# Kernel tuning notes

Measured on AMD Instinct MI355X. Metric: run time of the kernel, lower is better.

Reference implementation:

```python
import jax, jax.numpy as jnp
import numpy as np

NUM_HEADS = 16
B, S, H = 2, 8192, 1024


def setup_inputs() -> dict:
    key = jax.random.key(0)
    ks = jax.random.split(key, 6)
    scale = 1.0 / np.sqrt(H)
    return {
        "hidden_states": jax.random.normal(ks[0], (B, S, H), dtype=jnp.float32),
        "Wq": jax.random.normal(ks[1], (H, H), dtype=jnp.float32) * scale,
        "Wk": jax.random.normal(ks[2], (H, H), dtype=jnp.float32) * scale,
        "Wv": jax.random.normal(ks[3], (H, H), dtype=jnp.float32) * scale,
        "Wg": jax.random.normal(ks[4], (H, H), dtype=jnp.float32) * scale,
        "Wo": jax.random.normal(ks[5], (H, H), dtype=jnp.float32) * scale,
        "gamma": jnp.ones((H,), dtype=jnp.float32),
        "beta": jnp.zeros((H,), dtype=jnp.float32),
    }


def reference(hidden_states, Wq, Wk, Wv, Wg, Wo, gamma, beta):
    b, s, h = hidden_states.shape
    nh = NUM_HEADS
    dk = h // nh
    dv = h // nh
    # projections (bias-free linears)
    q = (hidden_states @ Wq).reshape(b, s, nh, dk)
    k = (hidden_states @ Wk).reshape(b, s, nh, dk)
    v = (hidden_states @ Wv).reshape(b, s, nh, dv)
    g = hidden_states @ Wg  # [b, s, h]
    # elu+1 feature map
    q = jax.nn.elu(q) + 1.0
    k = jax.nn.elu(k) + 1.0
    # kv = k outer v per token, then contracted with q  ==> (q.k) * v (no [b,h,n,d,e] tensor)
    qk = jnp.sum(q * k, axis=-1, keepdims=True)        # [b, s, nh, 1]
    k_sum = jnp.sum(k, axis=1, keepdims=True)          # [b, 1, nh, dk] (global over seq)
    normalizer = jnp.sum(q * k_sum, axis=-1, keepdims=True)  # [b, s, nh, 1]
    z = qk * v / (normalizer + 1e-6)                   # [b, s, nh, dv]
    z = z.reshape(b, s, nh * dv)
    # LayerNorm (eps=1e-5, affine)
    mu = jnp.mean(z, axis=-1, keepdims=True)
    var = jnp.mean(jnp.square(z - mu), axis=-1, keepdims=True)
    z = (z - mu) * jax.lax.rsqrt(var + 1e-5) * gamma + beta
    # SiLU gating and output projection
    z = z * jax.nn.silu(g)
    return z @ Wo
```

## Files before the change

kernel.cpp:

```cpp
#include <hip/hip_runtime.h>


typedef unsigned short ushort_t;
typedef unsigned int uint_t;

using short8  = __attribute__((ext_vector_type(8))) short;
using floatx4 = __attribute__((ext_vector_type(4))) float;

#define HDIM  1024
#define T_TOK 16384
#define KSPLIT 3072

__device__ __forceinline__ ushort_t f2bf(float f) {
    uint_t u = __builtin_bit_cast(uint_t, f);
    u = (u + 0x7fff + ((u >> 16) & 1)) >> 16;
    return (ushort_t)u;
}
__device__ __forceinline__ float bf2f(ushort_t h) {
    uint_t u = ((uint_t)h) << 16;
    return __builtin_bit_cast(float, u);
}
__device__ __forceinline__ void split2(float f, ushort_t& hi, ushort_t& lo) {
    hi = f2bf(f);
    lo = f2bf(f - bf2f(hi));
}
__device__ __forceinline__ void gload_lds16(const ushort_t* g, ushort_t* l) {
    __builtin_amdgcn_global_load_lds(
        (const __attribute__((address_space(1))) void*)g,
        (__attribute__((address_space(3))) void*)l, 16, 0, 0);
}

__global__ void split_w(const float* __restrict__ W0, const float* __restrict__ W1,
                        const float* __restrict__ W2, const float* __restrict__ W3,
                        const float* __restrict__ W4, ushort_t* __restrict__ WT2) {
    __shared__ float tile[32][33];
    const int z = blockIdx.z;
    const float* W = (z == 0) ? W0 : (z == 1) ? W1 : (z == 2) ? W2 : (z == 3) ? W3 : W4;
    ushort_t* dst = WT2 + (size_t)z * HDIM * 2048;
    const int n0 = blockIdx.x * 32, k0 = blockIdx.y * 32;
    const int tx = threadIdx.x & 31, ty0 = threadIdx.x >> 5;
#pragma unroll
    for (int s = 0; s < 4; ++s) {
        int ty = ty0 + 8 * s;
        tile[ty][tx] = W[(size_t)(k0 + ty) * HDIM + n0 + tx];
    }
    __syncthreads();
#pragma unroll
    for (int s = 0; s < 4; ++s) {
        int ty = ty0 + 8 * s;
        float v = tile[tx][ty];
        ushort_t hi, lo;
        split2(v, hi, lo);
        dst[(size_t)(n0 + ty) * 2048 + k0 + tx] = hi;
        dst[(size_t)(n0 + ty) * 2048 + 1024 + k0 + tx] = lo;
    }
}

__global__ __launch_bounds__(256)
void split_hidden(const float* __restrict__ h, ushort_t* __restrict__ Hs) {
    const int t = blockIdx.x;
    const int c = threadIdx.x;
    const float4 x = ((const float4*)(h + (size_t)t * HDIM))[c];
    ushort_t hi[4], lo[4];
    split2(x.x, hi[0], lo[0]); split2(x.y, hi[1], lo[1]);
    split2(x.z, hi[2], lo[2]); split2(x.w, hi[3], lo[3]);
    ushort_t* row = Hs + (size_t)t * 2048;
    uint2 hp, lp;
    hp.x = (uint_t)hi[0] | ((uint_t)hi[1] << 16);
    hp.y = (uint_t)hi[2] | ((uint_t)hi[3] << 16);
    lp.x = (uint_t)lo[0] | ((uint_t)lo[1] << 16);
    lp.y = (uint_t)lo[2] | ((uint_t)lo[3] << 16);
    *(uint2*)(row + c * 4) = hp;
    *(uint2*)(row + 1024 + c * 4) = lp;
}


#define FENCE() asm volatile("" ::: "memory")
#define BAR1()  do { FENCE(); __builtin_amdgcn_s_barrier(); FENCE(); \
                     __builtin_amdgcn_sched_barrier(0); } while (0)
#define BAR2()  do { FENCE(); __builtin_amdgcn_s_barrier(); FENCE(); } while (0)
#define VMW4()  asm volatile("s_waitcnt vmcnt(4)" ::: "memory")

#define STG_A(t, h, bsel) do { \
    const int ka_ = ((t) * 64 >= 2048) ? ((t) * 64 - 2048) : ((t) * 64); \
    gload_lds16(Ag + (size_t)((h) * 128) * 2048 + ka_, \
                &As[(bsel) * 16384 + ((h) * 128 + w * 16) * 64]); \
    gload_lds16(Ag + (size_t)((h) * 128 + 8) * 2048 + ka_, \
                &As[(bsel) * 16384 + ((h) * 128 + w * 16 + 8) * 64]); \
  } while (0)

#define STG_B(t, h, bsel) do { \
    const int kb_ = ((t) * 64 >= 1024) ? ((t) * 64 - 1024) : ((t) * 64); \
    gload_lds16(Bg + (size_t)((h) * 128) * 2048 + kb_, \
                &Bs[(bsel) * 16384 + ((h) * 128 + w * 16) * 64]); \
    gload_lds16(Bg + (size_t)((h) * 128 + 8) * 2048 + kb_, \
                &Bs[(bsel) * 16384 + ((h) * 128 + w * 16 + 8) * 64]); \
  } while (0)

#define RD_AF(p, bsel) do { \
    af[0][0] = *(const short8*)(Ar0 + (bsel) * 16384 + (2 * (p)) * 1024); \
    af[0][1] = *(const short8*)(Ar1 + (bsel) * 16384 + (2 * (p)) * 1024); \
    af[1][0] = *(const short8*)(Ar0 + (bsel) * 16384 + (2 * (p) + 1) * 1024); \
    af[1][1] = *(const short8*)(Ar1 + (bsel) * 16384 + (2 * (p) + 1) * 1024); \
  } while (0)

#define RD_BF(bsel) do { \
    _Pragma("unroll") \
    for (int j = 0; j < 4; ++j) { \
        bf[j][0] = *(const short8*)(Br0 + (bsel) * 16384 + j * 1024); \
        bf[j][1] = *(const short8*)(Br1 + (bsel) * 16384 + j * 1024); \
    } \
  } while (0)

#define MM(p) do { \
    __builtin_amdgcn_s_setprio(1); \
    _Pragma("unroll") \
    for (int di = 0; di < 2; ++di) \
    _Pragma("unroll") \
    for (int j = 0; j < 4; ++j) { \
        acc[2 * (p) + di][j] = __builtin_amdgcn_mfma_f32_16x16x32_bf16( \
            af[di][0], bf[j][0], acc[2 * (p) + di][j], 0, 0, 0); \
        acc[2 * (p) + di][j] = __builtin_amdgcn_mfma_f32_16x16x32_bf16( \
            af[di][1], bf[j][1], acc[2 * (p) + di][j], 0, 0, 0); \
    } \
    __builtin_amdgcn_s_setprio(0); \
  } while (0)

template <int EPI>
__global__ __launch_bounds__(512, 2)
void gemm256(const ushort_t* __restrict__ A, const ushort_t* __restrict__ Bw,
             float* __restrict__ D, const float* __restrict__ kf,
             const float* __restrict__ ksum, float* __restrict__ scbuf,
             ushort_t* __restrict__ zbuf, const float* __restrict__ gamma,
             const float* __restrict__ beta) {
    __shared__ ushort_t As[2 * 256 * 64];
    __shared__ ushort_t Bs[2 * 256 * 64];
    const int tid = threadIdx.x;
    const int bx = blockIdx.x, by = blockIdx.y;
    const int w = tid >> 6, lane = tid & 63;
    const int wm = w & 1, wn = w >> 1;
    const int lrow = lane & 15, lq = lane >> 4;

    const int srow = lane >> 3;
    const int scol = ((lane & 7) ^ srow) * 8;
    const ushort_t* Ag = A + (size_t)(bx * 256 + w * 16 + srow) * 2048 + scol;
    const ushort_t* Bg = Bw + (size_t)(by * 256 + w * 16 + srow) * 2048 + scol;

    const int c0 = (lq ^ (lrow & 7)) * 8;
    const int c1 = ((lq + 4) ^ (lrow & 7)) * 8;
    const ushort_t* Ar0 = As + (wm * 128 + lrow) * 64 + c0;
    const ushort_t* Ar1 = As + (wm * 128 + lrow) * 64 + c1;
    const ushort_t* Br0 = Bs + (wn * 64 + lrow) * 64 + c0;
    const ushort_t* Br1 = Bs + (wn * 64 + lrow) * 64 + c1;

    floatx4 acc[8][4] = {};
    short8 bf[4][2];
    short8 af[2][2];

    STG_A(0, 0, 0); STG_A(0, 1, 0);
    STG_B(0, 0, 0); STG_B(0, 1, 0);
    STG_B(1, 0, 1); STG_B(1, 1, 1);
    VMW4();
    BAR2();

#pragma unroll 1
    for (int t = 0; t < 48; t += 2) {
        RD_BF(0); RD_AF(0, 0);
        STG_A(t + 1, 0, 1); STG_A(t + 1, 1, 1);
        BAR1(); MM(0); BAR2();
        RD_AF(1, 0);
        STG_B(t + 2, 0, 0);
        BAR1(); MM(1); BAR2();
        RD_AF(2, 0);
        STG_B(t + 2, 1, 0);
        BAR1(); MM(2); BAR2();
        RD_AF(3, 0);
        BAR1(); MM(3);
        VMW4();
        BAR2();
        RD_BF(1); RD_AF(0, 1);
        STG_A(t + 2, 0, 0); STG_A(t + 2, 1, 0);
        BAR1(); MM(0); BAR2();
        RD_AF(1, 1);
        STG_B(t + 3, 0, 1);
        BAR1(); MM(1); BAR2();
        RD_AF(2, 1);
        STG_B(t + 3, 1, 1);
        BAR1(); MM(2); BAR2();
        RD_AF(3, 1);
        BAR1(); MM(3);
        VMW4();
        BAR2();
    }

    const int rowbase = bx * 256 + wm * 128 + lq * 4;
    const int colbase = by * 256 + wn * 64 + lrow;

    if constexpr (EPI == 0 || EPI == 2) {
#pragma unroll
        for (int i = 0; i < 8; ++i)
#pragma unroll
            for (int j = 0; j < 4; ++j) {
                const int col = colbase + j * 16;
#pragma unroll
                for (int r = 0; r < 4; ++r) {
                    const int row = rowbase + i * 16 + r;
                    float val = acc[i][j][r];
                    if (EPI == 0) val = (val > 0.0f) ? (val + 1.0f) : (expm1f(val) + 1.0f);
                    D[(size_t)row * HDIM + col] = val;
                }
            }
    } else if constexpr (EPI == 1) {
        const int b = bx >> 5;
        float ksv[4];
#pragma unroll
        for (int j = 0; j < 4; ++j) ksv[j] = ksum[b * HDIM + colbase + j * 16];
        const int h = by * 4 + wn;
#pragma unroll
        for (int i = 0; i < 8; ++i)
#pragma unroll
            for (int r = 0; r < 4; ++r) {
                const int row = rowbase + i * 16 + r;
                float qk = 0.f, nm = 0.f;
#pragma unroll
                for (int j = 0; j < 4; ++j) {
                    float qv = acc[i][j][r];
                    qv = (qv > 0.0f) ? (qv + 1.0f) : (expm1f(qv) + 1.0f);
                    const float kv = kf[(size_t)row * HDIM + colbase + j * 16];
                    qk += qv * kv;
                    nm += qv * ksv[j];
                }
#pragma unroll
                for (int off = 1; off < 16; off <<= 1) {
                    qk += __shfl_xor(qk, off, 64);
                    nm += __shfl_xor(nm, off, 64);
                }
                if (lrow == 0) scbuf[row * 16 + h] = qk / (nm + 1e-6f);
            }
    } else {
#pragma unroll
        for (int i = 0; i < 8; ++i)
#pragma unroll
            for (int j = 0; j < 4; ++j) {
                const int col = colbase + j * 16;
                const float gam = gamma[col], bet = beta[col];
#pragma unroll
                for (int r = 0; r < 4; ++r) {
                    const int row = rowbase + i * 16 + r;
                    ushort_t* zr = zbuf + (size_t)row * 2048;
                    const float zn = bf2f(zr[col]) + bf2f(zr[1024 + col]);
                    const float g = acc[i][j][r];
                    const float sg = g / (1.0f + expf(-g));
                    ushort_t hi, lo;
                    split2((zn * gam + bet) * sg, hi, lo);
                    zr[col] = hi;
                    zr[1024 + col] = lo;
                }
            }
    }
}

template <int EPI>
__global__ __launch_bounds__(256)
void gemm_swz(const ushort_t* __restrict__ A, const ushort_t* __restrict__ Bw,
              float* __restrict__ D, const float* __restrict__ kf,
              const float* __restrict__ ksum, float* __restrict__ scbuf,
              ushort_t* __restrict__ zbuf) {
    __shared__ ushort_t As[128 * 64];
    __shared__ ushort_t Bs[128 * 64];
    const int tid = threadIdx.x;
    const int bx = blockIdx.x, by = blockIdx.y;
    const int w = tid >> 6, lane = tid & 63;
    const int wm = w & 1, wn = w >> 1;
    const int lrow = lane & 15, lq = lane >> 4;

    const int srow = lane >> 3;
    const int scol = ((lane & 7) ^ srow) * 8;
    const ushort_t* Ag = A + (size_t)(bx * 128 + w * 32 + srow) * 2048 + scol;
    const ushort_t* Bg = Bw + (size_t)(by * 128 + w * 32 + srow) * 2048 + scol;

    floatx4 acc[4][4] = {};

    for (int k0 = 0; k0 < KSPLIT; k0 += 64) {
        const int ka = k0 - ((k0 >= 2048) ? 2048 : 0);
        const int kb = k0 - ((k0 >= 1024) ? 1024 : 0);
        __syncthreads();
#pragma unroll
        for (int n = 0; n < 4; ++n) {
            gload_lds16(Ag + (size_t)(n * 8) * 2048 + ka, &As[(w * 32 + n * 8) * 64]);
            gload_lds16(Bg + (size_t)(n * 8) * 2048 + kb, &Bs[(w * 32 + n * 8) * 64]);
        }
        __syncthreads();
#pragma unroll
        for (int kk = 0; kk < 64; kk += 32) {
            short8 af[4], bf[4];
#pragma unroll
            for (int i = 0; i < 4; ++i) {
                const int c = (((kk >> 3) + lq) ^ (lrow & 7)) * 8;
                af[i] = *(const short8*)&As[(wm * 64 + i * 16 + lrow) * 64 + c];
            }
#pragma unroll
            for (int j = 0; j < 4; ++j) {
                const int c = (((kk >> 3) + lq) ^ (lrow & 7)) * 8;
                bf[j] = *(const short8*)&Bs[(wn * 64 + j * 16 + lrow) * 64 + c];
            }
#pragma unroll
            for (int i = 0; i < 4; ++i)
#pragma unroll
                for (int j = 0; j < 4; ++j)
                    acc[i][j] = __builtin_amdgcn_mfma_f32_16x16x32_bf16(af[i], bf[j], acc[i][j], 0, 0, 0);
        }
    }

    const int rowbase = bx * 128 + wm * 64 + lq * 4;
    const int colbase = by * 128 + wn * 64 + lrow;
#pragma unroll
    for (int i = 0; i < 4; ++i)
#pragma unroll
        for (int j = 0; j < 4; ++j) {
            const int col = colbase + j * 16;
#pragma unroll
            for (int r = 0; r < 4; ++r) {
                const int row = rowbase + i * 16 + r;
                float val = acc[i][j][r];
                if (EPI == 0) val = (val > 0.0f) ? (val + 1.0f) : (expm1f(val) + 1.0f);
                D[(size_t)row * HDIM + col] = val;
            }
        }
}

__global__ void ksum_partial(const float* __restrict__ kf, float* __restrict__ partial) {
    const int rg = blockIdx.x;
    const int tid = threadIdx.x;
    const float4* p = (const float4*)(kf + (size_t)rg * 64 * HDIM) + tid;
    float4 s = {0.f, 0.f, 0.f, 0.f};
    for (int r = 0; r < 64; ++r) {
        float4 x = p[(size_t)r * (HDIM / 4)];
        s.x += x.x; s.y += x.y; s.z += x.z; s.w += x.w;
    }
    ((float4*)(partial + (size_t)rg * HDIM))[tid] = s;
}
__global__ void ksum_reduce(const float* __restrict__ partial, float* __restrict__ ksum) {
    const int b = blockIdx.y;
    const int c = blockIdx.x * 256 + threadIdx.x;
    float s = 0.f;
    const float* p = partial + (size_t)b * 128 * HDIM + c;
    for (int rg = 0; rg < 128; ++rg) s += p[(size_t)rg * HDIM];
    ksum[b * HDIM + c] = s;
}

__global__ __launch_bounds__(256)
void token_lite(float* vz, const float* __restrict__ scbuf) {
    const int t = blockIdx.x;
    const int tid = threadIdx.x;
    const float4 v = ((const float4*)(vz + (size_t)t * HDIM))[tid];
    const float sc = scbuf[t * 16 + (tid >> 4)];
    float z[4] = {v.x * sc, v.y * sc, v.z * sc, v.w * sc};

    __shared__ float red[8];
    const int wv = tid >> 6, lane = tid & 63;

    float s1 = z[0] + z[1] + z[2] + z[3];
#pragma unroll
    for (int off = 1; off < 64; off <<= 1) s1 += __shfl_xor(s1, off, 64);
    if (lane == 0) red[wv] = s1;
    __syncthreads();
    const float mu = (red[0] + red[1] + red[2] + red[3]) * (1.0f / 1024.0f);

    float d[4] = {z[0] - mu, z[1] - mu, z[2] - mu, z[3] - mu};
    float s2 = d[0] * d[0] + d[1] * d[1] + d[2] * d[2] + d[3] * d[3];
#pragma unroll
    for (int off = 1; off < 64; off <<= 1) s2 += __shfl_xor(s2, off, 64);
    __syncthreads();
    if (lane == 0) red[4 + wv] = s2;
    __syncthreads();
    const float var = (red[4] + red[5] + red[6] + red[7]) * (1.0f / 1024.0f);
    const float rstd = rsqrtf(var + 1e-5f);

    ushort_t* zrow = (ushort_t*)(vz + (size_t)t * HDIM);
    ushort_t hi[4], lo[4];
#pragma unroll
    for (int c = 0; c < 4; ++c) split2(d[c] * rstd, hi[c], lo[c]);
    uint2 hp, lp;
    hp.x = (uint_t)hi[0] | ((uint_t)hi[1] << 16);
    hp.y = (uint_t)hi[2] | ((uint_t)hi[3] << 16);
    lp.x = (uint_t)lo[0] | ((uint_t)lo[1] << 16);
    lp.y = (uint_t)lo[2] | ((uint_t)lo[3] << 16);
    *(uint2*)(zrow + tid * 4) = hp;
    *(uint2*)(zrow + 1024 + tid * 4) = lp;
}

template <int VAR>
__global__ __launch_bounds__(256, 2)
void gemm_split(const float* __restrict__ A,
                const ushort_t* __restrict__ B0, const ushort_t* __restrict__ B1,
                const ushort_t* __restrict__ B2,
                float* __restrict__ D0, float* __restrict__ D1, float* __restrict__ D2,
                int K) {
    __shared__ ushort_t Ah[128 * 72];
    __shared__ ushort_t Al[128 * 72];
    __shared__ ushort_t Bh[128 * 72];
    __shared__ ushort_t Bl[128 * 72];
    const int tid = threadIdx.x;
    const int bx = blockIdx.x, by = blockIdx.y;
    const ushort_t* Bt;
    float* D;
    int n0;
    bool act;
    if (VAR == 1) {
        const int wsel = by >> 3;
        Bt = (wsel == 0) ? B0 : (wsel == 1) ? B1 : B2;
        D = (wsel == 0) ? D0 : (wsel == 1) ? D1 : D2;
        n0 = (by & 7) * 128;
        act = (wsel == 0);
    } else {
        Bt = B0; D = D0; n0 = by * 128; act = true;
    }
    const int w = tid >> 6, lane = tid & 63;
    const int wm = w & 1, wn = w >> 1;
    const int lrow = lane & 15, lq = lane >> 4;
    const int srow = tid >> 1;
    const int shalf = (tid & 1) * 32;
    const float* Arow = A + (size_t)(bx * 128 + srow) * K;
    const ushort_t* Brow = Bt + (size_t)(n0 + srow) * 2048;
    floatx4 acc[4][4] = {};
    for (int k0 = 0; k0 < K; k0 += 64) {
        float4 afr[8];
        uint4 bhr[4], blr[4];
#pragma unroll
        for (int g = 0; g < 4; ++g) {
            afr[2 * g]     = *(const float4*)(Arow + k0 + shalf + g * 8);
            afr[2 * g + 1] = *(const float4*)(Arow + k0 + shalf + g * 8 + 4);
            bhr[g] = *(const uint4*)(Brow + k0 + shalf + g * 8);
            blr[g] = *(const uint4*)(Brow + 1024 + k0 + shalf + g * 8);
        }
        __syncthreads();
#pragma unroll
        for (int g = 0; g < 4; ++g) {
            ushort_t h[8], l[8];
            const float4 f0 = afr[2 * g], f1 = afr[2 * g + 1];
            split2(f0.x, h[0], l[0]); split2(f0.y, h[1], l[1]);
            split2(f0.z, h[2], l[2]); split2(f0.w, h[3], l[3]);
            split2(f1.x, h[4], l[4]); split2(f1.y, h[5], l[5]);
            split2(f1.z, h[6], l[6]); split2(f1.w, h[7], l[7]);
            uint4 hp, lp;
            hp.x = (uint_t)h[0] | ((uint_t)h[1] << 16);
            hp.y = (uint_t)h[2] | ((uint_t)h[3] << 16);
            hp.z = (uint_t)h[4] | ((uint_t)h[5] << 16);
            hp.w = (uint_t)h[6] | ((uint_t)h[7] << 16);
            lp.x = (uint_t)l[0] | ((uint_t)l[1] << 16);
            lp.y = (uint_t)l[2] | ((uint_t)l[3] << 16);
            lp.z = (uint_t)l[4] | ((uint_t)l[5] << 16);
            lp.w = (uint_t)l[6] | ((uint_t)l[7] << 16);
            *(uint4*)&Ah[srow * 72 + shalf + g * 8] = hp;
            *(uint4*)&Al[srow * 72 + shalf + g * 8] = lp;
            *(uint4*)&Bh[srow * 72 + shalf + g * 8] = bhr[g];
            *(uint4*)&Bl[srow * 72 + shalf + g * 8] = blr[g];
        }
        __syncthreads();
#pragma unroll
        for (int kk = 0; kk < 64; kk += 32) {
            short8 ah[4], bh[4], xl[4];
#pragma unroll
            for (int i = 0; i < 4; ++i)
                ah[i] = *(const short8*)&Ah[(wm * 64 + i * 16 + lrow) * 72 + kk + lq * 8];
#pragma unroll
            for (int j = 0; j < 4; ++j)
                bh[j] = *(const short8*)&Bh[(wn * 64 + j * 16 + lrow) * 72 + kk + lq * 8];
#pragma unroll
            for (int i = 0; i < 4; ++i)
#pragma unroll
                for (int j = 0; j < 4; ++j)
                    acc[i][j] = __builtin_amdgcn_mfma_f32_16x16x32_bf16(ah[i], bh[j], acc[i][j], 0, 0, 0);
#pragma unroll
            for (int i = 0; i < 4; ++i)
                xl[i] = *(const short8*)&Al[(wm * 64 + i * 16 + lrow) * 72 + kk + lq * 8];
#pragma unroll
            for (int i = 0; i < 4; ++i)
#pragma unroll
                for (int j = 0; j < 4; ++j)
                    acc[i][j] = __builtin_amdgcn_mfma_f32_16x16x32_bf16(xl[i], bh[j], acc[i][j], 0, 0, 0);
#pragma unroll
            for (int j = 0; j < 4; ++j)
                xl[j] = *(const short8*)&Bl[(wn * 64 + j * 16 + lrow) * 72 + kk + lq * 8];
#pragma unroll
            for (int i = 0; i < 4; ++i)
#pragma unroll
                for (int j = 0; j < 4; ++j)
                    acc[i][j] = __builtin_amdgcn_mfma_f32_16x16x32_bf16(ah[i], xl[j], acc[i][j], 0, 0, 0);
        }
    }
    const int rowbase = bx * 128 + wm * 64 + lq * 4;
    const int colbase = n0 + wn * 64 + lrow;
#pragma unroll
    for (int i = 0; i < 4; ++i)
#pragma unroll
        for (int j = 0; j < 4; ++j) {
            const int col = colbase + j * 16;
#pragma unroll
            for (int r = 0; r < 4; ++r) {
                const int row = rowbase + i * 16 + r;
                float val = acc[i][j][r];
                if (act) val = (val > 0.0f) ? (val + 1.0f) : (expm1f(val) + 1.0f);
                D[(size_t)row * HDIM + col] = val;
            }
        }
}

__global__ __launch_bounds__(256)
void token_f32(const float* __restrict__ qd, const float* __restrict__ vd,
               const float* __restrict__ gd, float* kz,
               const float* __restrict__ ksum,
               const float* __restrict__ gamma, const float* __restrict__ beta,
               int chunk_base) {
    const int tl = blockIdx.x;
    const int t = chunk_base + tl;
    const int b = t >> 13;
    const int tid = threadIdx.x;
    const float4 q = ((const float4*)(qd + (size_t)tl * HDIM))[tid];
    const float4 k = ((const float4*)(kz + (size_t)t * HDIM))[tid];
    const float4 v = ((const float4*)(vd + (size_t)tl * HDIM))[tid];
    const float4 ks = ((const float4*)(ksum + (size_t)b * HDIM))[tid];
    float qk = q.x * k.x + q.y * k.y + q.z * k.z + q.w * k.w;
    float nm = q.x * ks.x + q.y * ks.y + q.z * ks.z + q.w * ks.w;
#pragma unroll
    for (int off = 1; off < 16; off <<= 1) {
        qk += __shfl_xor(qk, off, 64);
        nm += __shfl_xor(nm, off, 64);
    }
    const float sc = qk / (nm + 1e-6f);
    float z[4] = {v.x * sc, v.y * sc, v.z * sc, v.w * sc};
    __shared__ float red[8];
    const int wv = tid >> 6, lane = tid & 63;
    float s1 = z[0] + z[1] + z[2] + z[3];
#pragma unroll
    for (int off = 1; off < 64; off <<= 1) s1 += __shfl_xor(s1, off, 64);
    if (lane == 0) red[wv] = s1;
    __syncthreads();
    const float mu = (red[0] + red[1] + red[2] + red[3]) * (1.0f / 1024.0f);
    float d[4] = {z[0] - mu, z[1] - mu, z[2] - mu, z[3] - mu};
    float s2 = d[0] * d[0] + d[1] * d[1] + d[2] * d[2] + d[3] * d[3];
#pragma unroll
    for (int off = 1; off < 64; off <<= 1) s2 += __shfl_xor(s2, off, 64);
    __syncthreads();
    if (lane == 0) red[4 + wv] = s2;
    __syncthreads();
    const float var = (red[4] + red[5] + red[6] + red[7]) * (1.0f / 1024.0f);
    const float rstd = rsqrtf(var + 1e-5f);
    const float4 gm = ((const float4*)gamma)[tid];
    const float4 bt = ((const float4*)beta)[tid];
    const float4 g = ((const float4*)(gd + (size_t)tl * HDIM))[tid];
    const float gv[4] = {g.x, g.y, g.z, g.w};
    const float gmv[4] = {gm.x, gm.y, gm.z, gm.w};
    const float btv[4] = {bt.x, bt.y, bt.z, bt.w};
    ushort_t hi[4], lo[4];
#pragma unroll
    for (int c = 0; c < 4; ++c) {
        const float zn = d[c] * rstd * gmv[c] + btv[c];
        const float sg = gv[c] / (1.0f + expf(-gv[c]));
        split2(zn * sg, hi[c], lo[c]);
    }
    ushort_t* zrow = (ushort_t*)(kz + (size_t)t * HDIM);
    uint2 hp, lp;
    hp.x = (uint_t)hi[0] | ((uint_t)hi[1] << 16);
    hp.y = (uint_t)hi[2] | ((uint_t)hi[3] << 16);
    lp.x = (uint_t)lo[0] | ((uint_t)lo[1] << 16);
    lp.y = (uint_t)lo[2] | ((uint_t)lo[3] << 16);
    *(uint2*)(zrow + tid * 4) = hp;
    *(uint2*)(zrow + 1024 + tid * 4) = lp;
}

extern "C" void kernel_launch(void* const* d_in, const int* in_sizes, int n_in,
                              void* d_out, int out_size, void* d_ws, size_t ws_size,
                              hipStream_t stream) {
    const float* hidden = (const float*)d_in[0];
    const float* Wq = (const float*)d_in[1];
    const float* Wk = (const float*)d_in[2];
    const float* Wv = (const float*)d_in[3];
    const float* Wg = (const float*)d_in[4];
    const float* Wo = (const float*)d_in[5];
    const float* gamma = (const float*)d_in[6];
    const float* beta = (const float*)d_in[7];

    char* w = (char*)d_ws;
    float* kb = (float*)w;            w += (size_t)67108864;
    ushort_t* WT2 = (ushort_t*)w;     w += (size_t)20971520;
    float* partial = (float*)w;       w += (size_t)1048576;
    float* ksum = (float*)w;          w += (size_t)8192;
    float* scbuf = (float*)w;         w += (size_t)1048576;
    const size_t base = (size_t)(w - (char*)d_ws);

    ushort_t* Wk2 = WT2;
    ushort_t* Wq2 = WT2 + (size_t)1 * HDIM * 2048;
    ushort_t* Wv2 = WT2 + (size_t)2 * HDIM * 2048;
    ushort_t* Wg2 = WT2 + (size_t)3 * HDIM * 2048;
    ushort_t* Wo2 = WT2 + (size_t)4 * HDIM * 2048;

    split_w<<<dim3(32, 32, 5), 256, 0, stream>>>(Wk, Wq, Wv, Wg, Wo, WT2);

    if (ws_size >= base + 67108864ull) {
        ushort_t* Hs = (ushort_t*)w;
        split_hidden<<<dim3(T_TOK), 256, 0, stream>>>(hidden, Hs);
        gemm256<0><<<dim3(64, 4), 512, 0, stream>>>(Hs, Wk2, kb, nullptr, nullptr,
                                                    nullptr, nullptr, nullptr, nullptr);
        ksum_partial<<<dim3(256), 256, 0, stream>>>(kb, partial);
        ksum_reduce<<<dim3(4, 2), 256, 0, stream>>>(partial, ksum);
        gemm256<1><<<dim3(64, 4), 512, 0, stream>>>(Hs, Wq2, nullptr, kb, ksum,
                                                    scbuf, nullptr, nullptr, nullptr);
        gemm256<2><<<dim3(64, 4), 512, 0, stream>>>(Hs, Wv2, kb, nullptr, nullptr,
                                                    nullptr, nullptr, nullptr, nullptr);
        token_lite<<<dim3(T_TOK), 256, 0, stream>>>(kb, scbuf);
        gemm256<3><<<dim3(64, 4), 512, 0, stream>>>(Hs, Wg2, nullptr, nullptr, nullptr,
                                                    nullptr, (ushort_t*)kb, gamma, beta);
        gemm256<2><<<dim3(64, 4), 512, 0, stream>>>((const ushort_t*)kb, Wo2,
                                                    (float*)d_out, nullptr, nullptr,
                                                    nullptr, nullptr, nullptr, nullptr);
    } else {
        const int C = 2048;
        float* qc = (float*)w;
        float* vc = qc + (size_t)C * HDIM;
        float* gc = vc + (size_t)C * HDIM;
        gemm_split<0><<<dim3(128, 8), 256, 0, stream>>>(hidden, Wk2, nullptr, nullptr,
                                                        kb, nullptr, nullptr, HDIM);
        ksum_partial<<<dim3(256), 256, 0, stream>>>(kb, partial);
        ksum_reduce<<<dim3(4, 2), 256, 0, stream>>>(partial, ksum);
        for (int c = 0; c < 8; ++c) {
            const float* Ac = hidden + (size_t)c * C * HDIM;
            gemm_split<1><<<dim3(C / 128, 24), 256, 0, stream>>>(Ac, Wq2, Wv2, Wg2,
                                                                 qc, vc, gc, HDIM);
            token_f32<<<dim3(C), 256, 0, stream>>>(qc, vc, gc, kb, ksum,
                                                   gamma, beta, c * C);
        }
        gemm_swz<2><<<dim3(128, 8), 256, 0, stream>>>((const ushort_t*)kb, Wo2,
                                                      (float*)d_out, nullptr, nullptr,
                                                      nullptr, nullptr);
    }
}
```

Before: 679.0 us.

## Software-pipeline GEMM fragment loads with register double buffering and fewer barriers

Restructures the bf16 GEMM main loop so LDS fragment reads for the next k-chunk and row block go into alternate register sets (afA/afB, bfv0/bfv1) while MFMAs run on the current set. The loop drops from eight workgroup barriers per k-tile to two, placed around the B-tile staging. The aim is to cut barrier stalls and hide LDS latency behind matrix math. In exchange it needs more fragment registers, which could raise register pressure, and it relies on the new read and stage ordering to avoid LDS hazards.

```diff
diff --git a/kernel.cpp b/kernel.cpp
--- a/kernel.cpp
+++ b/kernel.cpp
@@ -76,9 +76,6 @@
 
 
 #define FENCE() asm volatile("" ::: "memory")
-#define BAR1()  do { FENCE(); __builtin_amdgcn_s_barrier(); FENCE(); \
-                     __builtin_amdgcn_sched_barrier(0); } while (0)
-#define BAR2()  do { FENCE(); __builtin_amdgcn_s_barrier(); FENCE(); } while (0)
 #define VMW4()  asm volatile("s_waitcnt vmcnt(4)" ::: "memory")
 
 #define STG_A(t, h, bsel) do { \
@@ -97,33 +94,55 @@
                 &Bs[(bsel) * 16384 + ((h) * 128 + w * 16 + 8) * 64]); \
   } while (0)
 
-#define RD_AF(p, bsel) do { \
-    af[0][0] = *(const short8*)(Ar0 + (bsel) * 16384 + (2 * (p)) * 1024); \
-    af[0][1] = *(const short8*)(Ar1 + (bsel) * 16384 + (2 * (p)) * 1024); \
-    af[1][0] = *(const short8*)(Ar0 + (bsel) * 16384 + (2 * (p) + 1) * 1024); \
-    af[1][1] = *(const short8*)(Ar1 + (bsel) * 16384 + (2 * (p) + 1) * 1024); \
+#define RD_A(dst, bsel, mb, kc) do { \
+    const ushort_t* _pa = ((kc) ? Ar1 : Ar0) + (bsel) * 16384; \
+    _Pragma("unroll") \
+    for (int _i = 0; _i < 4; ++_i) \
+        dst[_i] = *(const short8*)(_pa + ((mb) + _i) * 1024); \
   } while (0)
 
-#define RD_BF(bsel) do { \
+#define RD_B(dst, bsel, kc) do { \
+    const ushort_t* _pb = ((kc) ? Br1 : Br0) + (bsel) * 16384; \
     _Pragma("unroll") \
-    for (int j = 0; j < 4; ++j) { \
-        bf[j][0] = *(const short8*)(Br0 + (bsel) * 16384 + j * 1024); \
-        bf[j][1] = *(const short8*)(Br1 + (bsel) * 16384 + j * 1024); \
-    } \
+    for (int _j = 0; _j < 4; ++_j) \
+        dst[_j] = *(const short8*)(_pb + _j * 1024); \
   } while (0)
 
-#define MM(p) do { \
+#define MMX(mb, a, b) do { \
     __builtin_amdgcn_s_setprio(1); \
     _Pragma("unroll") \
-    for (int di = 0; di < 2; ++di) \
+    for (int _i = 0; _i < 4; ++_i) \
     _Pragma("unroll") \
-    for (int j = 0; j < 4; ++j) { \
-        acc[2 * (p) + di][j] = __builtin_amdgcn_mfma_f32_16x16x32_bf16( \
-            af[di][0], bf[j][0], acc[2 * (p) + di][j], 0, 0, 0); \
-        acc[2 * (p) + di][j] = __builtin_amdgcn_mfma_f32_16x16x32_bf16( \
-            af[di][1], bf[j][1], acc[2 * (p) + di][j], 0, 0, 0); \
-    } \
+    for (int _j = 0; _j < 4; ++_j) \
+        acc[(mb) + _i][_j] = __builtin_amdgcn_mfma_f32_16x16x32_bf16( \
+            a[_i], b[_j], acc[(mb) + _i][_j], 0, 0, 0); \
     __builtin_amdgcn_s_setprio(0); \
+  } while (0)
+
+#define TILE(t, bsel) do { \
+     \
+    RD_A(afB, bsel, 4, 0); \
+    STG_A((t) + 1, 0, (bsel) ^ 1); STG_A((t) + 1, 1, (bsel) ^ 1); \
+    MMX(0, afA, bfv0); \
+     \
+    RD_A(afA, bsel, 0, 1); \
+    RD_B(bfv1, bsel, 1); \
+    MMX(4, afB, bfv0); \
+     \
+    RD_A(afB, bsel, 4, 1); \
+    MMX(0, afA, bfv1); \
+     \
+    __builtin_amdgcn_sched_barrier(0); \
+    asm volatile("s_waitcnt lgkmcnt(0)" ::: "memory"); \
+    FENCE(); __builtin_amdgcn_s_barrier(); FENCE(); \
+    STG_B((t) + 2, 0, bsel); STG_B((t) + 2, 1, bsel); \
+    VMW4(); \
+    FENCE(); __builtin_amdgcn_s_barrier(); FENCE(); \
+    __builtin_amdgcn_sched_barrier(0); \
+     \
+    RD_A(afA, (bsel) ^ 1, 0, 0); \
+    RD_B(bfv0, (bsel) ^ 1, 0); \
+    MMX(4, afB, bfv1); \
   } while (0)
 
 template <int EPI>
@@ -154,43 +173,21 @@
     const ushort_t* Br1 = Bs + (wn * 64 + lrow) * 64 + c1;
 
     floatx4 acc[8][4] = {};
-    short8 bf[4][2];
-    short8 af[2][2];
+    short8 afA[4], afB[4], bfv0[4], bfv1[4];
 
     STG_A(0, 0, 0); STG_A(0, 1, 0);
     STG_B(0, 0, 0); STG_B(0, 1, 0);
     STG_B(1, 0, 1); STG_B(1, 1, 1);
     VMW4();
-    BAR2();
+    FENCE(); __builtin_amdgcn_s_barrier(); FENCE();
+    __builtin_amdgcn_sched_barrier(0);
+    RD_A(afA, 0, 0, 0);
+    RD_B(bfv0, 0, 0);
 
 #pragma unroll 1
     for (int t = 0; t < 48; t += 2) {
-        RD_BF(0); RD_AF(0, 0);
-        STG_A(t + 1, 0, 1); STG_A(t + 1, 1, 1);
-        BAR1(); MM(0); BAR2();
-        RD_AF(1, 0);
-        STG_B(t + 2, 0, 0);
-        BAR1(); MM(1); BAR2();
-        RD_AF(2, 0);
-        STG_B(t + 2, 1, 0);
-        BAR1(); MM(2); BAR2();
-        RD_AF(3, 0);
-        BAR1(); MM(3);
-        VMW4();
-        BAR2();
-        RD_BF(1); RD_AF(0, 1);
-        STG_A(t + 2, 0, 0); STG_A(t + 2, 1, 0);
-        BAR1(); MM(0); BAR2();
-        RD_AF(1, 1);
-        STG_B(t + 3, 0, 1);
-        BAR1(); MM(1); BAR2();
-        RD_AF(2, 1);
-        STG_B(t + 3, 1, 1);
-        BAR1(); MM(2); BAR2();
-        RD_AF(3, 1);
-        BAR1(); MM(3);
-        VMW4();
-        BAR2();
+        TILE(t, 0);
+        TILE(t + 1, 1);
     }
 
     const int rowbase = bx * 256 + wm * 128 + lq * 4;
```

Result: slower. 693.9 us (+2.2%).
